# Performance work log

Measured on AMD Instinct MI355X. Metric: run time of the kernel, lower is better.

## Reference

```python
import jax, jax.numpy as jnp
import numpy as np

B, S, C = 4096, 6, 2048  # batch, num_strips, in_channel
D = C // 8               # query/key projection dim

def setup_inputs() -> dict:
    key = jax.random.key(0)
    k1, k2, k3, k4 = jax.random.split(key, 4)
    sc = 1.0 / np.sqrt(C)
    return {
        "x": jax.random.normal(k1, (B, S, C), dtype=jnp.float32),
        "Wq": jax.random.normal(k2, (D, C), dtype=jnp.float32) * sc,
        "Wk": jax.random.normal(k3, (D, C), dtype=jnp.float32) * sc,
        "Wv": jax.random.normal(k4, (C, C), dtype=jnp.float32) * sc,
        "gamma": jnp.ones((1,), dtype=jnp.float32),
    }

def reference(x, Wq, Wk, Wv, gamma):
    # x: [B, S, C] stacked squeezed strips (feat in the torch code)
    q = jnp.einsum('bsc,dc->bsd', x, Wq)          # [B, S, D]
    k = jnp.einsum('bsc,dc->bsd', x, Wk)          # [B, S, D]
    energy = jnp.einsum('bsd,btd->bst', q, k)     # [B, S, S]
    attention = jax.nn.softmax(energy, axis=-1)   # softmax over keys
    v = jnp.einsum('bsc,dc->bsd', x, Wv)          # [B, S, C]
    out = jnp.einsum('bst,btc->bsc', attention, v)  # [B, S, C]
    out = gamma * out + x                         # gamma-scaled residual
    return out, attention
```

## Files before the change

kernel.cpp:

```cpp
#include <hip/hip_runtime.h>

typedef __attribute__((ext_vector_type(4))) float f32x4;
typedef __attribute__((ext_vector_type(8))) _Float16 f16x8;
typedef __attribute__((ext_vector_type(4))) unsigned short u16x4;
typedef __attribute__((ext_vector_type(8))) unsigned short u16x8;

#define NB 4096
#define NS 6
#define NC 2048
#define MTOT (NB * NS)

static __device__ __forceinline__ unsigned short f2h_bits(float f) {
  _Float16 h = (_Float16)f;
  unsigned short b;
  __builtin_memcpy(&b, &h, 2);
  return b;
}
static __device__ __forceinline__ float h2f(unsigned short b) {
  _Float16 h;
  __builtin_memcpy(&h, &b, 2);
  return (float)h;
}

__global__ void conv_f16_kernel(const float* __restrict__ in,
                                unsigned short* __restrict__ out, int n4) {
  int i = blockIdx.x * blockDim.x + threadIdx.x;
  const int stride = gridDim.x * blockDim.x;
  for (; i < n4; i += stride) {
    f32x4 v = reinterpret_cast<const f32x4*>(in)[i];
    u16x4 o;
#pragma unroll
    for (int j = 0; j < 4; ++j) o[j] = f2h_bits(v[j]);
    reinterpret_cast<u16x4*>(out)[i] = o;
  }
}

__global__ void prep_wqk_kernel(const float* __restrict__ Wq,
                                const float* __restrict__ Wk,
                                unsigned short* __restrict__ w) {
  int i = blockIdx.x * blockDim.x + threadIdx.x;
  const int stride = gridDim.x * blockDim.x;
  for (; i < 262144; i += stride) {
    const int row = i >> 9;
    const int col4 = i & 511;
    const float* src = (row < 256) ? (Wq + (size_t)row * NC)
                                   : (Wk + (size_t)(row - 256) * NC);
    f32x4 v = reinterpret_cast<const f32x4*>(src)[col4];
    u16x4 o;
#pragma unroll
    for (int j = 0; j < 4; ++j) o[j] = f2h_bits(v[j]);
    reinterpret_cast<u16x4*>(w)[i] = o;
  }
}


#define FENCE() asm volatile("" ::: "memory")
#define BAR() do { FENCE(); __builtin_amdgcn_s_barrier(); FENCE(); } while (0)
#define VM4BAR() do { FENCE(); asm volatile("s_waitcnt vmcnt(4)" ::: "memory"); \
                      __builtin_amdgcn_s_barrier(); FENCE(); } while (0)

template <int MB>
__device__ __forceinline__ void mfma_blk(f32x4 (&acc)[8][4], const f16x8 (&Av)[4],
                                         const f16x8 (&Bv)[4]) {
  __builtin_amdgcn_s_setprio(1);
#pragma unroll
  for (int m = 0; m < 4; ++m)
#pragma unroll
    for (int n = 0; n < 4; ++n)
      acc[MB + m][n] =
          __builtin_amdgcn_mfma_f32_16x16x32_f16(Av[m], Bv[n], acc[MB + m][n], 0, 0, 0);
  __builtin_amdgcn_s_setprio(0);
}

__device__ __forceinline__ void load4(f16x8 (&dst)[4], const char* base, int kk) {
#pragma unroll
  for (int m = 0; m < 4; ++m)
    dst[m] = *reinterpret_cast<const f16x8*>(base + (m * 2 + kk) * 1024);
}

__device__ __forceinline__ void stage_op(const unsigned short* g, int row0, int k0,
                                         char* ldsOp, int wid, int lane) {
  const int sl = lane ^ ((lane >> 4) & 1) ^ (((lane >> 5) & 1) << 1);
#pragma unroll
  for (int h = 0; h < 2; ++h)
#pragma unroll
    for (int i = 0; i < 2; ++i) {
      const int c = wid * 2 + i;
      const unsigned short* src =
          g + (size_t)(row0 + h * 128 + (c >> 1) * 16 + (sl >> 2)) * 2048 +
          (unsigned)(k0 + (c & 1) * 32 + (sl & 3) * 8);
      __builtin_amdgcn_global_load_lds(
          (__attribute__((address_space(1))) void*)src,
          (__attribute__((address_space(3))) void*)(ldsOp + h * 16384 + c * 1024),
          16, 0, 0);
    }
}

template <int NSEG, int N, bool EPI, bool NFAST>
__global__ void __launch_bounds__(512, 2)
gemm256(const unsigned short* __restrict__ A0, const unsigned short* __restrict__ B0,
        const unsigned short* __restrict__ A1, const unsigned short* __restrict__ B1,
        float* __restrict__ C, const float* __restrict__ resid,
        const float* __restrict__ gam) {
  constexpr int NTPS = 2048 / 64;
  constexpr int NT = NSEG * NTPS;
  constexpr int MT = MTOT / 256;
  constexpr int NXT = N / 256;
  constexpr int NWG = MT * NXT;
  constexpr int CPX = NWG / 8;
  __shared__ char lds[131072];

  const int bid = blockIdx.x;
  const int wg = (bid & 7) * CPX + (bid >> 3);
  const int bx = NFAST ? (wg % NXT) : (wg / MT);
  const int by = NFAST ? (wg / NXT) : (wg % MT);
  const int m0 = by * 256, n0 = bx * 256;

  const int t = threadIdx.x;
  const int lane = t & 63;
  const int wid = t >> 6;
  const int wr = wid >> 2, wc = wid & 3;
  const int laneOff = (lane & 15) * 64 + (lane >> 4) * 16;
  const int swzOff = laneOff ^ (((laneOff >> 9) & 1) << 5) ^ (((laneOff >> 8) & 1) << 4);

  f32x4 acc[8][4] = {};
  f16x8 A03[4], A47[4], Bk0[4], Bk1[4];

  const int aBase = wr * 16384 + swzOff;
  const int bBase = 32768 + (wc >> 1) * 16384 + (wc & 1) * 8192 + swzOff;

#define SEL(P0, P1, S) ((NSEG == 1) ? (P0) : ((S) == 0 ? (P0) : (P1)))
#define WRAPT(TT) ((TT) >= NT ? (TT) - NT : (TT))
#define STAGE_A(TT) do { int tw_ = WRAPT(TT); int s_ = tw_ / NTPS; \
    stage_op(SEL(A0, A1, s_), m0, (tw_ % NTPS) * 64, lds + ((TT) & 1) * 65536, wid, lane); } while (0)
#define STAGE_B(TT) do { int tw_ = WRAPT(TT); int s_ = tw_ / NTPS; \
    stage_op(SEL(B0, B1, s_), n0, (tw_ % NTPS) * 64, lds + ((TT) & 1) * 65536 + 32768, wid, lane); } while (0)

  STAGE_A(0);
  STAGE_B(0);
  STAGE_B(1);
  VM4BAR();

#define TILE(TAU, FIRST) do { \
    char* bufc = lds + ((TAU) & 1) * 65536; \
     \
    load4(A03, bufc + aBase, 0); \
    load4(Bk0, bufc + bBase, 0); \
    STAGE_A((TAU) + 1); \
    BAR(); \
    if (!(FIRST)) mfma_blk<4>(acc, A47, Bk1); \
    BAR(); \
     \
    load4(A47, bufc + aBase + 8192, 0); \
    BAR(); \
    mfma_blk<0>(acc, A03, Bk0); \
    BAR(); \
     \
    load4(A03, bufc + aBase, 1); \
    load4(Bk1, bufc + bBase, 1); \
    BAR(); \
    mfma_blk<4>(acc, A47, Bk0); \
    BAR(); \
     \
    load4(A47, bufc + aBase + 8192, 1); \
    STAGE_B((TAU) + 2); \
    VM4BAR(); \
    mfma_blk<0>(acc, A03, Bk1); \
    BAR(); \
  } while (0)

  TILE(0, 1);
  for (int tau = 1; tau < NT; ++tau) TILE(tau, 0);
  mfma_blk<4>(acc, A47, Bk1);

#undef TILE
#undef STAGE_A
#undef STAGE_B
#undef WRAPT
#undef SEL

  const float g = EPI ? gam[0] : 0.f;
#pragma unroll
  for (int m = 0; m < 8; ++m)
#pragma unroll
    for (int n = 0; n < 4; ++n)
#pragma unroll
      for (int j = 0; j < 4; ++j) {
        const int r = m0 + wr * 128 + m * 16 + (lane >> 4) * 4 + j;
        const int c = n0 + wc * 64 + n * 16 + (lane & 15);
        const size_t idx = (size_t)r * (size_t)N + (size_t)c;
        float v = acc[m][n][j];
        if (EPI) v = g * v + resid[idx];
        C[idx] = v;
      }
}

__global__ void __launch_bounds__(256)
attn_fuse(const float* __restrict__ QK,
          const unsigned short* __restrict__ xh,
          float* __restrict__ attn_out,
          unsigned short* __restrict__ y)
{
  __shared__ float qk[NS * 512];
  __shared__ float eng[36];
  __shared__ float att[36];
  const int b = blockIdx.x;
  const int t = threadIdx.x;
  {
    const f32x4* src = reinterpret_cast<const f32x4*>(QK + (size_t)b * (NS * 512));
    f32x4* dst = reinterpret_cast<f32x4*>(qk);
    for (int i = t; i < (NS * 512) / 4; i += 256) dst[i] = src[i];
  }
  __syncthreads();
  if (t < 144) {
    const int s = t / 24;
    const int rem = t - s * 24;
    const int u = rem >> 2;
    const int sub = rem & 3;
    const float* qr = qk + s * 512;
    const float* kr = qk + u * 512 + 256;
    float sum = 0.f;
    const int d0 = sub * 64;
#pragma unroll 4
    for (int d = 0; d < 64; ++d) sum += qr[d0 + d] * kr[d0 + d];
    sum += __shfl_xor(sum, 1);
    sum += __shfl_xor(sum, 2);
    if (sub == 0) eng[s * 6 + u] = sum;
  }
  __syncthreads();
  if (t < 6) {
    float e[6];
#pragma unroll
    for (int u = 0; u < 6; ++u) e[u] = eng[t * 6 + u];
    float mx = e[0];
#pragma unroll
    for (int u = 1; u < 6; ++u) mx = fmaxf(mx, e[u]);
    float p[6];
    float sm = 0.f;
#pragma unroll
    for (int u = 0; u < 6; ++u) { p[u] = expf(e[u] - mx); sm += p[u]; }
    const float inv = 1.0f / sm;
#pragma unroll
    for (int u = 0; u < 6; ++u) {
      const float a = p[u] * inv;
      att[t * 6 + u] = a;
      attn_out[(size_t)b * 36 + t * 6 + u] = a;
    }
  }
  __syncthreads();
  const unsigned short* xb = xh + (size_t)b * (NS * NC);
  unsigned short* yb = y + (size_t)b * (NS * NC);
  const int c0 = t * 8;
  f32x4 xv[12];
#pragma unroll
  for (int u = 0; u < 6; ++u) {
    u16x8 v = *reinterpret_cast<const u16x8*>(xb + u * NC + c0);
#pragma unroll
    for (int j = 0; j < 4; ++j) {
      xv[2 * u][j] = h2f(v[j]);
      xv[2 * u + 1][j] = h2f(v[4 + j]);
    }
  }
#pragma unroll
  for (int s = 0; s < 6; ++s) {
    f32x4 a0 = 0.f, a1 = 0.f;
#pragma unroll
    for (int u = 0; u < 6; ++u) {
      const float w = att[s * 6 + u];
      a0 += w * xv[2 * u];
      a1 += w * xv[2 * u + 1];
    }
    u16x8 o;
#pragma unroll
    for (int j = 0; j < 4; ++j) { o[j] = f2h_bits(a0[j]); o[4 + j] = f2h_bits(a1[j]); }
    *reinterpret_cast<u16x8*>(yb + s * NC + c0) = o;
  }
}

extern "C" void kernel_launch(void* const* d_in, const int* in_sizes, int n_in,
                              void* d_out, int out_size, void* d_ws, size_t ws_size,
                              hipStream_t stream) {
  (void)in_sizes; (void)n_in; (void)out_size; (void)ws_size;
  const float* x   = (const float*)d_in[0];
  const float* Wq  = (const float*)d_in[1];
  const float* Wk  = (const float*)d_in[2];
  const float* Wv  = (const float*)d_in[3];
  const float* gam = (const float*)d_in[4];
  float* out = (float*)d_out;
  float* attn_out = out + (size_t)MTOT * NC;

  char* ws = (char*)d_ws;
  unsigned short* xh  = (unsigned short*)(ws);
  unsigned short* yb  = (unsigned short*)(ws + 100663296ull);
  unsigned short* wqk = (unsigned short*)(ws + 201326592ull);
  unsigned short* wvh = (unsigned short*)(ws + 203423744ull);
  float*          qkb = (float*)(ws + 211812352ull);

  conv_f16_kernel<<<2048, 256, 0, stream>>>(x, xh, MTOT * NC / 4);
  prep_wqk_kernel<<<256, 256, 0, stream>>>(Wq, Wk, wqk);
  conv_f16_kernel<<<512, 256, 0, stream>>>(Wv, wvh, NC * NC / 4);

  gemm256<1, 512, false, false><<<192, 512, 0, stream>>>(
      xh, wqk, nullptr, nullptr, qkb, nullptr, nullptr);

  attn_fuse<<<NB, 256, 0, stream>>>(qkb, xh, attn_out, yb);

  gemm256<1, 2048, true, true><<<768, 512, 0, stream>>>(
      yb, wvh, nullptr, nullptr, out, x, gam);
}
```

Before: 421.1 us.

## Replace 256x256 pipelined GEMM with simpler 128x128 double-buffered GEMM

Swaps the 256x256-tile, 512-thread GEMM, which interleaves LDS fragment loads with MFMA blocks, for a 128x128-tile, 256-thread kernel with a K-step of 32 and a plain double buffer that waits for all loads to finish (vmcnt(0)) each iteration. LDS use per block drops from 128KB to 32KB and launch bounds allow 4 blocks per CU, so occupancy rises and both GEMMs run with four times as many workgroups. The cost is less operand reuse per tile, which means more global and LDS traffic per flop, plus a full barrier and load drain on every step with no software pipelining.

```diff
diff --git a/kernel.cpp b/kernel.cpp
--- a/kernel.cpp
+++ b/kernel.cpp
@@ -55,138 +55,91 @@
 
 
 #define FENCE() asm volatile("" ::: "memory")
-#define BAR() do { FENCE(); __builtin_amdgcn_s_barrier(); FENCE(); } while (0)
-#define VM4BAR() do { FENCE(); asm volatile("s_waitcnt vmcnt(4)" ::: "memory"); \
+#define VM0BAR() do { FENCE(); asm volatile("s_waitcnt vmcnt(0)" ::: "memory"); \
                       __builtin_amdgcn_s_barrier(); FENCE(); } while (0)
 
-template <int MB>
-__device__ __forceinline__ void mfma_blk(f32x4 (&acc)[8][4], const f16x8 (&Av)[4],
-                                         const f16x8 (&Bv)[4]) {
-  __builtin_amdgcn_s_setprio(1);
-#pragma unroll
-  for (int m = 0; m < 4; ++m)
-#pragma unroll
-    for (int n = 0; n < 4; ++n)
-      acc[MB + m][n] =
-          __builtin_amdgcn_mfma_f32_16x16x32_f16(Av[m], Bv[n], acc[MB + m][n], 0, 0, 0);
-  __builtin_amdgcn_s_setprio(0);
-}
-
-__device__ __forceinline__ void load4(f16x8 (&dst)[4], const char* base, int kk) {
-#pragma unroll
-  for (int m = 0; m < 4; ++m)
-    dst[m] = *reinterpret_cast<const f16x8*>(base + (m * 2 + kk) * 1024);
-}
-
-__device__ __forceinline__ void stage_op(const unsigned short* g, int row0, int k0,
-                                         char* ldsOp, int wid, int lane) {
+__device__ __forceinline__ void stage128(const unsigned short* gA,
+                                         const unsigned short* gB, int m0, int n0,
+                                         int k0, char* buf, int wid, int lane) {
   const int sl = lane ^ ((lane >> 4) & 1) ^ (((lane >> 5) & 1) << 1);
-#pragma unroll
-  for (int h = 0; h < 2; ++h)
-#pragma unroll
-    for (int i = 0; i < 2; ++i) {
-      const int c = wid * 2 + i;
-      const unsigned short* src =
-          g + (size_t)(row0 + h * 128 + (c >> 1) * 16 + (sl >> 2)) * 2048 +
-          (unsigned)(k0 + (c & 1) * 32 + (sl & 3) * 8);
-      __builtin_amdgcn_global_load_lds(
-          (__attribute__((address_space(1))) void*)src,
-          (__attribute__((address_space(3))) void*)(ldsOp + h * 16384 + c * 1024),
-          16, 0, 0);
-    }
-}
-
-template <int NSEG, int N, bool EPI, bool NFAST>
-__global__ void __launch_bounds__(512, 2)
-gemm256(const unsigned short* __restrict__ A0, const unsigned short* __restrict__ B0,
-        const unsigned short* __restrict__ A1, const unsigned short* __restrict__ B1,
+  const int rr = sl >> 2;
+  const int kc = (sl & 3) * 8;
+#pragma unroll
+  for (int i = 0; i < 2; ++i) {
+    const int c = wid * 2 + i;
+    const unsigned short* sA = gA + (size_t)(m0 + c * 16 + rr) * 2048 + (k0 + kc);
+    __builtin_amdgcn_global_load_lds(
+        (__attribute__((address_space(1))) void*)sA,
+        (__attribute__((address_space(3))) void*)(buf + c * 1024), 16, 0, 0);
+    const unsigned short* sB = gB + (size_t)(n0 + c * 16 + rr) * 2048 + (k0 + kc);
+    __builtin_amdgcn_global_load_lds(
+        (__attribute__((address_space(1))) void*)sB,
+        (__attribute__((address_space(3))) void*)(buf + 8192 + c * 1024), 16, 0, 0);
+  }
+}
+
+template <int N, bool EPI, bool NFAST>
+__global__ void __launch_bounds__(256, 4)
+gemm128(const unsigned short* __restrict__ A, const unsigned short* __restrict__ B,
         float* __restrict__ C, const float* __restrict__ resid,
         const float* __restrict__ gam) {
-  constexpr int NTPS = 2048 / 64;
-  constexpr int NT = NSEG * NTPS;
-  constexpr int MT = MTOT / 256;
-  constexpr int NXT = N / 256;
+  constexpr int NT = 64;
+  constexpr int MT = MTOT / 128;
+  constexpr int NXT = N / 128;
   constexpr int NWG = MT * NXT;
   constexpr int CPX = NWG / 8;
-  __shared__ char lds[131072];
+  __shared__ char lds[32768];
 
   const int bid = blockIdx.x;
   const int wg = (bid & 7) * CPX + (bid >> 3);
   const int bx = NFAST ? (wg % NXT) : (wg / MT);
   const int by = NFAST ? (wg / NXT) : (wg % MT);
-  const int m0 = by * 256, n0 = bx * 256;
+  const int m0 = by * 128, n0 = bx * 128;
 
   const int t = threadIdx.x;
   const int lane = t & 63;
   const int wid = t >> 6;
-  const int wr = wid >> 2, wc = wid & 3;
+  const int wr = wid >> 1, wc = wid & 1;
   const int laneOff = (lane & 15) * 64 + (lane >> 4) * 16;
   const int swzOff = laneOff ^ (((laneOff >> 9) & 1) << 5) ^ (((laneOff >> 8) & 1) << 4);
-
-  f32x4 acc[8][4] = {};
-  f16x8 A03[4], A47[4], Bk0[4], Bk1[4];
-
-  const int aBase = wr * 16384 + swzOff;
-  const int bBase = 32768 + (wc >> 1) * 16384 + (wc & 1) * 8192 + swzOff;
-
-#define SEL(P0, P1, S) ((NSEG == 1) ? (P0) : ((S) == 0 ? (P0) : (P1)))
-#define WRAPT(TT) ((TT) >= NT ? (TT) - NT : (TT))
-#define STAGE_A(TT) do { int tw_ = WRAPT(TT); int s_ = tw_ / NTPS; \
-    stage_op(SEL(A0, A1, s_), m0, (tw_ % NTPS) * 64, lds + ((TT) & 1) * 65536, wid, lane); } while (0)
-#define STAGE_B(TT) do { int tw_ = WRAPT(TT); int s_ = tw_ / NTPS; \
-    stage_op(SEL(B0, B1, s_), n0, (tw_ % NTPS) * 64, lds + ((TT) & 1) * 65536 + 32768, wid, lane); } while (0)
-
-  STAGE_A(0);
-  STAGE_B(0);
-  STAGE_B(1);
-  VM4BAR();
-
-#define TILE(TAU, FIRST) do { \
-    char* bufc = lds + ((TAU) & 1) * 65536; \
-     \
-    load4(A03, bufc + aBase, 0); \
-    load4(Bk0, bufc + bBase, 0); \
-    STAGE_A((TAU) + 1); \
-    BAR(); \
-    if (!(FIRST)) mfma_blk<4>(acc, A47, Bk1); \
-    BAR(); \
-     \
-    load4(A47, bufc + aBase + 8192, 0); \
-    BAR(); \
-    mfma_blk<0>(acc, A03, Bk0); \
-    BAR(); \
-     \
-    load4(A03, bufc + aBase, 1); \
-    load4(Bk1, bufc + bBase, 1); \
-    BAR(); \
-    mfma_blk<4>(acc, A47, Bk0); \
-    BAR(); \
-     \
-    load4(A47, bufc + aBase + 8192, 1); \
-    STAGE_B((TAU) + 2); \
-    VM4BAR(); \
-    mfma_blk<0>(acc, A03, Bk1); \
-    BAR(); \
-  } while (0)
-
-  TILE(0, 1);
-  for (int tau = 1; tau < NT; ++tau) TILE(tau, 0);
-  mfma_blk<4>(acc, A47, Bk1);
-
-#undef TILE
-#undef STAGE_A
-#undef STAGE_B
-#undef WRAPT
-#undef SEL
+  const int aBase = wr * 4096 + swzOff;
+  const int bBase = 8192 + wc * 4096 + swzOff;
+
+  f32x4 acc[4][4] = {};
+
+#define STAGE(TT) stage128(A, B, m0, n0, (TT) * 32, lds + ((TT) & 1) * 16384, wid, lane)
+
+  STAGE(0);
+
+  for (int tau = 0; tau < NT; ++tau) {
+    VM0BAR();
+    if (tau + 1 < NT) STAGE(tau + 1);
+    const char* bufc = lds + (tau & 1) * 16384;
+    f16x8 Af[4], Bf[4];
+#pragma unroll
+    for (int m = 0; m < 4; ++m)
+      Af[m] = *reinterpret_cast<const f16x8*>(bufc + aBase + m * 1024);
+#pragma unroll
+    for (int n = 0; n < 4; ++n)
+      Bf[n] = *reinterpret_cast<const f16x8*>(bufc + bBase + n * 1024);
+    __builtin_amdgcn_s_setprio(1);
+#pragma unroll
+    for (int m = 0; m < 4; ++m)
+#pragma unroll
+      for (int n = 0; n < 4; ++n)
+        acc[m][n] = __builtin_amdgcn_mfma_f32_16x16x32_f16(Af[m], Bf[n], acc[m][n], 0, 0, 0);
+    __builtin_amdgcn_s_setprio(0);
+  }
+#undef STAGE
 
   const float g = EPI ? gam[0] : 0.f;
 #pragma unroll
-  for (int m = 0; m < 8; ++m)
+  for (int m = 0; m < 4; ++m)
 #pragma unroll
     for (int n = 0; n < 4; ++n)
 #pragma unroll
       for (int j = 0; j < 4; ++j) {
-        const int r = m0 + wr * 128 + m * 16 + (lane >> 4) * 4 + j;
+        const int r = m0 + wr * 64 + m * 16 + (lane >> 4) * 4 + j;
         const int c = n0 + wc * 64 + n * 16 + (lane & 15);
         const size_t idx = (size_t)r * (size_t)N + (size_t)c;
         float v = acc[m][n][j];
@@ -300,11 +253,11 @@
   prep_wqk_kernel<<<256, 256, 0, stream>>>(Wq, Wk, wqk);
   conv_f16_kernel<<<512, 256, 0, stream>>>(Wv, wvh, NC * NC / 4);
 
-  gemm256<1, 512, false, false><<<192, 512, 0, stream>>>(
-      xh, wqk, nullptr, nullptr, qkb, nullptr, nullptr);
+  gemm128<512, false, false><<<768, 256, 0, stream>>>(
+      xh, wqk, qkb, nullptr, nullptr);
 
   attn_fuse<<<NB, 256, 0, stream>>>(qkb, xh, attn_out, yb);
 
-  gemm256<1, 2048, true, true><<<768, 512, 0, stream>>>(
-      yb, wvh, nullptr, nullptr, out, x, gam);
-}
+  gemm128<2048, true, true><<<3072, 256, 0, stream>>>(
+      yb, wvh, out, x, gam);
+}
```

After: 481.3 us. +14.3%, slower.

## Simplify GEMM main loop schedule and fuse fp16 conversion kernels

Applied to the files above, without the earlier changes.

Replaces the interleaved 8-barrier-per-tile GEMM schedule, in which LDS fragment loads alternate with MFMA half-blocks, with a simpler loop. Each k-tile now loads all A/B fragments for one k-half, issues 32 MFMAs, loads the second half, and uses two barriers per tile. This cuts barrier count, but it raises register pressure and removes the overlap between LDS reads and MFMA work. It also merges the three fp32-to-fp16 conversion kernels into one launch to save launch overhead, and drops the unused two-segment template support.

```diff
diff --git a/kernel.cpp b/kernel.cpp
--- a/kernel.cpp
+++ b/kernel.cpp
@@ -22,34 +22,39 @@
   return (float)h;
 }
 
-__global__ void conv_f16_kernel(const float* __restrict__ in,
-                                unsigned short* __restrict__ out, int n4) {
-  int i = blockIdx.x * blockDim.x + threadIdx.x;
-  const int stride = gridDim.x * blockDim.x;
-  for (; i < n4; i += stride) {
-    f32x4 v = reinterpret_cast<const f32x4*>(in)[i];
+#define NX4 12582912
+#define NW4 262144
+#define NV4 1048576
+__global__ void prep_all(const float* __restrict__ x, const float* __restrict__ Wq,
+                         const float* __restrict__ Wk, const float* __restrict__ Wv,
+                         unsigned short* __restrict__ xh, unsigned short* __restrict__ wqk,
+                         unsigned short* __restrict__ wvh) {
+  long i = blockIdx.x * blockDim.x + threadIdx.x;
+  const long stride = (long)gridDim.x * blockDim.x;
+  for (; i < NX4 + NW4 + NV4; i += stride) {
+    f32x4 v;
+    unsigned short* dst;
+    long di;
+    if (i < NX4) {
+      v = reinterpret_cast<const f32x4*>(x)[i];
+      dst = xh; di = i;
+    } else if (i < NX4 + NW4) {
+      const long j = i - NX4;
+      const int row = (int)(j >> 9);
+      const int col4 = (int)(j & 511);
+      const float* src = (row < 256) ? (Wq + (size_t)row * NC)
+                                     : (Wk + (size_t)(row - 256) * NC);
+      v = reinterpret_cast<const f32x4*>(src)[col4];
+      dst = wqk; di = j;
+    } else {
+      const long j = i - NX4 - NW4;
+      v = reinterpret_cast<const f32x4*>(Wv)[j];
+      dst = wvh; di = j;
+    }
     u16x4 o;
 #pragma unroll
     for (int j = 0; j < 4; ++j) o[j] = f2h_bits(v[j]);
-    reinterpret_cast<u16x4*>(out)[i] = o;
-  }
-}
-
-__global__ void prep_wqk_kernel(const float* __restrict__ Wq,
-                                const float* __restrict__ Wk,
-                                unsigned short* __restrict__ w) {
-  int i = blockIdx.x * blockDim.x + threadIdx.x;
-  const int stride = gridDim.x * blockDim.x;
-  for (; i < 262144; i += stride) {
-    const int row = i >> 9;
-    const int col4 = i & 511;
-    const float* src = (row < 256) ? (Wq + (size_t)row * NC)
-                                   : (Wk + (size_t)(row - 256) * NC);
-    f32x4 v = reinterpret_cast<const f32x4*>(src)[col4];
-    u16x4 o;
-#pragma unroll
-    for (int j = 0; j < 4; ++j) o[j] = f2h_bits(v[j]);
-    reinterpret_cast<u16x4*>(w)[i] = o;
+    reinterpret_cast<u16x4*>(dst)[di] = o;
   }
 }
 
@@ -58,25 +63,6 @@
 #define BAR() do { FENCE(); __builtin_amdgcn_s_barrier(); FENCE(); } while (0)
 #define VM4BAR() do { FENCE(); asm volatile("s_waitcnt vmcnt(4)" ::: "memory"); \
                       __builtin_amdgcn_s_barrier(); FENCE(); } while (0)
-
-template <int MB>
-__device__ __forceinline__ void mfma_blk(f32x4 (&acc)[8][4], const f16x8 (&Av)[4],
-                                         const f16x8 (&Bv)[4]) {
-  __builtin_amdgcn_s_setprio(1);
-#pragma unroll
-  for (int m = 0; m < 4; ++m)
-#pragma unroll
-    for (int n = 0; n < 4; ++n)
-      acc[MB + m][n] =
-          __builtin_amdgcn_mfma_f32_16x16x32_f16(Av[m], Bv[n], acc[MB + m][n], 0, 0, 0);
-  __builtin_amdgcn_s_setprio(0);
-}
-
-__device__ __forceinline__ void load4(f16x8 (&dst)[4], const char* base, int kk) {
-#pragma unroll
-  for (int m = 0; m < 4; ++m)
-    dst[m] = *reinterpret_cast<const f16x8*>(base + (m * 2 + kk) * 1024);
-}
 
 __device__ __forceinline__ void stage_op(const unsigned short* g, int row0, int k0,
                                          char* ldsOp, int wid, int lane) {
@@ -96,14 +82,12 @@
     }
 }
 
-template <int NSEG, int N, bool EPI, bool NFAST>
+template <int N, bool EPI, bool NFAST>
 __global__ void __launch_bounds__(512, 2)
-gemm256(const unsigned short* __restrict__ A0, const unsigned short* __restrict__ B0,
-        const unsigned short* __restrict__ A1, const unsigned short* __restrict__ B1,
+gemm256(const unsigned short* __restrict__ A, const unsigned short* __restrict__ B,
         float* __restrict__ C, const float* __restrict__ resid,
         const float* __restrict__ gam) {
-  constexpr int NTPS = 2048 / 64;
-  constexpr int NT = NSEG * NTPS;
+  constexpr int NT = 2048 / 64;
   constexpr int MT = MTOT / 256;
   constexpr int NXT = N / 256;
   constexpr int NWG = MT * NXT;
@@ -122,62 +106,64 @@
   const int wr = wid >> 2, wc = wid & 3;
   const int laneOff = (lane & 15) * 64 + (lane >> 4) * 16;
   const int swzOff = laneOff ^ (((laneOff >> 9) & 1) << 5) ^ (((laneOff >> 8) & 1) << 4);
-
-  f32x4 acc[8][4] = {};
-  f16x8 A03[4], A47[4], Bk0[4], Bk1[4];
-
   const int aBase = wr * 16384 + swzOff;
   const int bBase = 32768 + (wc >> 1) * 16384 + (wc & 1) * 8192 + swzOff;
 
-#define SEL(P0, P1, S) ((NSEG == 1) ? (P0) : ((S) == 0 ? (P0) : (P1)))
+  f32x4 acc[8][4] = {};
+
 #define WRAPT(TT) ((TT) >= NT ? (TT) - NT : (TT))
-#define STAGE_A(TT) do { int tw_ = WRAPT(TT); int s_ = tw_ / NTPS; \
-    stage_op(SEL(A0, A1, s_), m0, (tw_ % NTPS) * 64, lds + ((TT) & 1) * 65536, wid, lane); } while (0)
-#define STAGE_B(TT) do { int tw_ = WRAPT(TT); int s_ = tw_ / NTPS; \
-    stage_op(SEL(B0, B1, s_), n0, (tw_ % NTPS) * 64, lds + ((TT) & 1) * 65536 + 32768, wid, lane); } while (0)
+#define STAGE_A(TT) stage_op(A, m0, WRAPT(TT) * 64, lds + ((TT) & 1) * 65536, wid, lane)
+#define STAGE_B(TT) stage_op(B, n0, WRAPT(TT) * 64, lds + ((TT) & 1) * 65536 + 32768, wid, lane)
 
   STAGE_A(0);
   STAGE_B(0);
   STAGE_B(1);
   VM4BAR();
 
-#define TILE(TAU, FIRST) do { \
-    char* bufc = lds + ((TAU) & 1) * 65536; \
-     \
-    load4(A03, bufc + aBase, 0); \
-    load4(Bk0, bufc + bBase, 0); \
-    STAGE_A((TAU) + 1); \
-    BAR(); \
-    if (!(FIRST)) mfma_blk<4>(acc, A47, Bk1); \
-    BAR(); \
-     \
-    load4(A47, bufc + aBase + 8192, 0); \
-    BAR(); \
-    mfma_blk<0>(acc, A03, Bk0); \
-    BAR(); \
-     \
-    load4(A03, bufc + aBase, 1); \
-    load4(Bk1, bufc + bBase, 1); \
-    BAR(); \
-    mfma_blk<4>(acc, A47, Bk0); \
-    BAR(); \
-     \
-    load4(A47, bufc + aBase + 8192, 1); \
-    STAGE_B((TAU) + 2); \
-    VM4BAR(); \
-    mfma_blk<0>(acc, A03, Bk1); \
-    BAR(); \
-  } while (0)
-
-  TILE(0, 1);
-  for (int tau = 1; tau < NT; ++tau) TILE(tau, 0);
-  mfma_blk<4>(acc, A47, Bk1);
-
-#undef TILE
+  for (int tau = 0; tau < NT; ++tau) {
+    char* bufc = lds + (tau & 1) * 65536;
+    STAGE_A(tau + 1);
+    f16x8 Af[8], Bf[4];
+#pragma unroll
+    for (int m = 0; m < 4; ++m) {
+      Af[m]     = *reinterpret_cast<const f16x8*>(bufc + aBase + (m * 2) * 1024);
+      Af[4 + m] = *reinterpret_cast<const f16x8*>(bufc + aBase + 8192 + (m * 2) * 1024);
+    }
+#pragma unroll
+    for (int n = 0; n < 4; ++n)
+      Bf[n] = *reinterpret_cast<const f16x8*>(bufc + bBase + (n * 2) * 1024);
+    __builtin_amdgcn_s_setprio(1);
+#pragma unroll
+    for (int m = 0; m < 8; ++m)
+#pragma unroll
+      for (int n = 0; n < 4; ++n)
+        acc[m][n] = __builtin_amdgcn_mfma_f32_16x16x32_f16(Af[m], Bf[n], acc[m][n], 0, 0, 0);
+    __builtin_amdgcn_s_setprio(0);
+    f16x8 Ag[8], Bg[4];
+#pragma unroll
+    for (int m = 0; m < 4; ++m) {
+      Ag[m]     = *reinterpret_cast<const f16x8*>(bufc + aBase + (m * 2 + 1) * 1024);
+      Ag[4 + m] = *reinterpret_cast<const f16x8*>(bufc + aBase + 8192 + (m * 2 + 1) * 1024);
+    }
+#pragma unroll
+    for (int n = 0; n < 4; ++n)
+      Bg[n] = *reinterpret_cast<const f16x8*>(bufc + bBase + (n * 2 + 1) * 1024);
+    BAR();
+    STAGE_B(tau + 2);
+    VM4BAR();
+    __builtin_amdgcn_s_setprio(1);
+#pragma unroll
+    for (int m = 0; m < 8; ++m)
+#pragma unroll
+      for (int n = 0; n < 4; ++n)
+        acc[m][n] = __builtin_amdgcn_mfma_f32_16x16x32_f16(Ag[m], Bg[n], acc[m][n], 0, 0, 0);
+    __builtin_amdgcn_s_setprio(0);
+    BAR();
+  }
+
 #undef STAGE_A
 #undef STAGE_B
 #undef WRAPT
-#undef SEL
 
   const float g = EPI ? gam[0] : 0.f;
 #pragma unroll
@@ -296,15 +282,13 @@
   unsigned short* wvh = (unsigned short*)(ws + 203423744ull);
   float*          qkb = (float*)(ws + 211812352ull);
 
-  conv_f16_kernel<<<2048, 256, 0, stream>>>(x, xh, MTOT * NC / 4);
-  prep_wqk_kernel<<<256, 256, 0, stream>>>(Wq, Wk, wqk);
-  conv_f16_kernel<<<512, 256, 0, stream>>>(Wv, wvh, NC * NC / 4);
-
-  gemm256<1, 512, false, false><<<192, 512, 0, stream>>>(
-      xh, wqk, nullptr, nullptr, qkb, nullptr, nullptr);
+  prep_all<<<2048, 256, 0, stream>>>(x, Wq, Wk, Wv, xh, wqk, wvh);
+
+  gemm256<512, false, false><<<192, 512, 0, stream>>>(
+      xh, wqk, qkb, nullptr, nullptr);
 
   attn_fuse<<<NB, 256, 0, stream>>>(qkb, xh, attn_out, yb);
 
-  gemm256<1, 2048, true, true><<<768, 512, 0, stream>>>(
-      yb, wvh, nullptr, nullptr, out, x, gam);
-}
+  gemm256<2048, true, true><<<768, 512, 0, stream>>>(
+      yb, wvh, out, x, gam);
+}
```

New measurement: 407.9 us. -3.1%, faster.
